# Kernel optimization log

Hardware: AMD Instinct MI355X
Metric: run time of the kernel (lower is better)

Reference implementation:

```python
import jax, jax.numpy as jnp
import numpy as np

EMBEDDING_LENGTH = 2048
EMBEDDING_DIM = 4


def setup_inputs() -> dict:
    key = jax.random.key(0)
    kx, ke = jax.random.split(key)
    x = jax.random.uniform(kx, (16, 64, 64, EMBEDDING_DIM), dtype=jnp.float32)
    embedding = jax.random.uniform(ke, (EMBEDDING_LENGTH, EMBEDDING_DIM), dtype=jnp.float32)
    return {"x": x, "embedding": embedding}


def reference(x, embedding):
    # x: [B, w, h, c], embedding: [K, c]
    B, w, h, c = x.shape
    flat = x.reshape(-1, c)  # [N, c], N = B*w*h
    # ||f - e||^2 = ||f||^2 - 2 f.e + ||e||^2 (avoids materializing [N, K, c])
    x2 = jnp.sum(flat * flat, axis=-1, keepdims=True)          # [N, 1]
    e2 = jnp.sum(embedding * embedding, axis=-1)               # [K]
    dots = jnp.einsum('nc,kc->nk', flat, embedding)            # [N, K]
    dists = x2 - 2.0 * dots + e2                               # [N, K]
    idx = jnp.argmin(dists, axis=-1)                           # [N] int
    return idx.reshape(B, w, h)
```

## Files before the change

kernel.cpp:

```cpp
#include <hip/hip_runtime.h>
#include <math.h>

#pragma clang fp contract(off)

typedef __attribute__((ext_vector_type(2))) float f2;

constexpr int KCODES = 2048;
constexpr int CDIM   = 4;
constexpr int KSPLIT = 8;
constexpr int KCHUNK = KCODES / KSPLIT;
constexpr int ROWS   = 64;
constexpr int NUNITS = KCODES / 2;

__device__ __forceinline__ f2 pk_mul(f2 a, f2 b) {
    f2 d; asm("v_pk_mul_f32 %0, %1, %2" : "=v"(d) : "v"(a), "v"(b)); return d;
}
__device__ __forceinline__ f2 pk_fma(f2 a, f2 b, f2 c) {
    f2 d; asm("v_pk_fma_f32 %0, %1, %2, %3" : "=v"(d) : "v"(a), "v"(b), "v"(c)); return d;
}
__device__ __forceinline__ f2 pk_add(f2 a, f2 b) {
    f2 d; asm("v_pk_add_f32 %0, %1, %2" : "=v"(d) : "v"(a), "v"(b)); return d;
}
__device__ __forceinline__ float min3f(float a, float b, float c) {
    float d; asm("v_min3_f32 %0, %1, %2, %3" : "=v"(d) : "v"(a), "v"(b), "v"(c)); return d;
}

__device__ __forceinline__ float sumsq(float4 e) {
    return ((e.x * e.x + e.y * e.y) + e.z * e.z) + e.w * e.w;
}

__global__ __launch_bounds__(512, 4) void vq_fused(
    const float* __restrict__ x,
    const float* __restrict__ emb,
    int* __restrict__ out,
    int N)
{
    __shared__ float4 sEP[NUNITS * 2];
    __shared__ float4 sSP[KCODES / 4];

    const float4* __restrict__ embf4 = reinterpret_cast<const float4*>(emb);
    const int t = threadIdx.x;

    for (int j = t; j < NUNITS; j += 512) {
        float4 a = embf4[2 * j], b = embf4[2 * j + 1];
        sEP[2 * j]     = make_float4(a.x, b.x, a.y, b.y);
        sEP[2 * j + 1] = make_float4(a.z, b.z, a.w, b.w);
    }
    for (int q = t; q < KCODES / 4; q += 512) {
        float4 e0 = embf4[4 * q], e1 = embf4[4 * q + 1];
        float4 e2 = embf4[4 * q + 2], e3 = embf4[4 * q + 3];
        sSP[q] = make_float4(sumsq(e0), sumsq(e1), sumsq(e2), sumsq(e3));
    }
    __syncthreads();

    const int lane = t & 63;
    const int n    = blockIdx.x * ROWS + lane;
    const int wid   = __builtin_amdgcn_readfirstlane(t >> 6);
    const int kbase = wid * KCHUNK;
    const int ubase = kbase >> 1;
    const int qbase = kbase >> 2;

    unsigned long long key = ~0ull;
    if (n < N) {
        const float4 xv = reinterpret_cast<const float4*>(x)[n];
        const float x2 = ((xv.x * xv.x + xv.y * xv.y) + xv.z * xv.z) + xv.w * xv.w;
        const f2 xx = {xv.x, xv.x}, yy = {xv.y, xv.y};
        const f2 zz = {xv.z, xv.z}, ww = {xv.w, xv.w};
        const f2 x2p = {x2, x2};
        const f2 m2  = {-2.0f, -2.0f};

        float dmin = HUGE_VALF;
        int bg = 0;

        for (int g = 0; g < KCHUNK / 8; ++g) {
            const float prev = dmin;
            const float4 sA = sSP[qbase + 2 * g];
            const float4 sB = sSP[qbase + 2 * g + 1];
            const int u0 = ubase + 4 * g;
            #pragma unroll
            for (int uu = 0; uu < 4; ++uu) {
                const float4 qa = sEP[2 * (u0 + uu)];
                const float4 qb = sEP[2 * (u0 + uu) + 1];
                const f2 sp = (uu == 0) ? f2{sA.x, sA.y} :
                              (uu == 1) ? f2{sA.z, sA.w} :
                              (uu == 2) ? f2{sB.x, sB.y} : f2{sB.z, sB.w};
                f2 dot = pk_mul(xx, f2{qa.x, qa.y});
                dot = pk_fma(yy, f2{qa.z, qa.w}, dot);
                dot = pk_fma(zz, f2{qb.x, qb.y}, dot);
                dot = pk_fma(ww, f2{qb.z, qb.w}, dot);
                f2 dd = pk_add(pk_fma(m2, dot, x2p), sp);
                dmin = min3f(dmin, dd.x, dd.y);
            }
            if (dmin < prev) bg = g;
        }

        const int k0 = kbase + (bg << 3);
        int idx = 0x7fffffff;
        #pragma unroll
        for (int r = 0; r < 8; ++r) {
            const int k = k0 + r;
            const float4 e = embf4[k];
            const float s = sumsq(e);
            float dot = xv.x * e.x;
            dot = __builtin_fmaf(xv.y, e.y, dot);
            dot = __builtin_fmaf(xv.z, e.z, dot);
            dot = __builtin_fmaf(xv.w, e.w, dot);
            const float d = __builtin_fmaf(-2.0f, dot, x2) + s;
            idx = min(idx, (d == dmin) ? k : 0x7fffffff);
        }

        key = ((unsigned long long)__float_as_uint(dmin) << 32) | (unsigned)idx;
    }

    __syncthreads();
    unsigned long long* skey = reinterpret_cast<unsigned long long*>(sEP);
    skey[lane * (KSPLIT + 1) + wid] = key;
    __syncthreads();

    if (t < ROWS) {
        const int rn = blockIdx.x * ROWS + t;
        if (rn < N) {
            unsigned long long k = skey[t * (KSPLIT + 1)];
            #pragma unroll
            for (int s = 1; s < KSPLIT; ++s) {
                unsigned long long v = skey[t * (KSPLIT + 1) + s];
                if (v < k) k = v;
            }
            out[rn] = (int)(unsigned)(k & 0xFFFFFFFFull);
        }
    }
}

extern "C" void kernel_launch(void* const* d_in, const int* in_sizes, int n_in,
                              void* d_out, int out_size, void* d_ws, size_t ws_size,
                              hipStream_t stream) {
    const float* x   = (const float*)d_in[0];
    const float* emb = (const float*)d_in[1];
    int* out = (int*)d_out;
    const int N = in_sizes[0] / CDIM;

    vq_fused<<<(N + ROWS - 1) / ROWS, 512, 0, stream>>>(x, emb, out, N);
}
```

Measured before the change: 30.59 us.

## Process four rows per thread to reuse codebook LDS loads

```diff
diff --git a/kernel.cpp b/kernel.cpp
--- a/kernel.cpp
+++ b/kernel.cpp
@@ -9,7 +9,8 @@
 constexpr int CDIM   = 4;
 constexpr int KSPLIT = 8;
 constexpr int KCHUNK = KCODES / KSPLIT;
-constexpr int ROWS   = 64;
+constexpr int RPT    = 4;
+constexpr int ROWSPB = 64 * RPT;
 constexpr int NUNITS = KCODES / 2;
 
 __device__ __forceinline__ f2 pk_mul(f2 a, f2 b) {
@@ -29,7 +30,7 @@
     return ((e.x * e.x + e.y * e.y) + e.z * e.z) + e.w * e.w;
 }
 
-__global__ __launch_bounds__(512, 4) void vq_fused(
+__global__ __launch_bounds__(512) void vq_fused(
     const float* __restrict__ x,
     const float* __restrict__ emb,
     int* __restrict__ out,
@@ -47,78 +48,98 @@
         sEP[2 * j + 1] = make_float4(a.z, b.z, a.w, b.w);
     }
     for (int q = t; q < KCODES / 4; q += 512) {
-        float4 e0 = embf4[4 * q], e1 = embf4[4 * q + 1];
+        float4 e0 = embf4[4 * q],     e1 = embf4[4 * q + 1];
         float4 e2 = embf4[4 * q + 2], e3 = embf4[4 * q + 3];
         sSP[q] = make_float4(sumsq(e0), sumsq(e1), sumsq(e2), sumsq(e3));
     }
     __syncthreads();
 
     const int lane = t & 63;
-    const int n    = blockIdx.x * ROWS + lane;
     const int wid   = __builtin_amdgcn_readfirstlane(t >> 6);
     const int kbase = wid * KCHUNK;
     const int ubase = kbase >> 1;
     const int qbase = kbase >> 2;
+    const int nbase = blockIdx.x * ROWSPB + lane;
 
-    unsigned long long key = ~0ull;
-    if (n < N) {
-        const float4 xv = reinterpret_cast<const float4*>(x)[n];
-        const float x2 = ((xv.x * xv.x + xv.y * xv.y) + xv.z * xv.z) + xv.w * xv.w;
-        const f2 xx = {xv.x, xv.x}, yy = {xv.y, xv.y};
-        const f2 zz = {xv.z, xv.z}, ww = {xv.w, xv.w};
-        const f2 x2p = {x2, x2};
-        const f2 m2  = {-2.0f, -2.0f};
+    float4 xv[RPT];
+    f2 xx[RPT], yy[RPT], zz[RPT], ww[RPT], x2p[RPT];
+    float dmin[RPT];
+    int   bg[RPT];
+    #pragma unroll
+    for (int r = 0; r < RPT; ++r) {
+        const int n = nbase + r * 64;
+        xv[r] = (n < N) ? reinterpret_cast<const float4*>(x)[n]
+                        : make_float4(0.f, 0.f, 0.f, 0.f);
+        const float x2 = ((xv[r].x * xv[r].x + xv[r].y * xv[r].y)
+                          + xv[r].z * xv[r].z) + xv[r].w * xv[r].w;
+        xx[r] = f2{xv[r].x, xv[r].x}; yy[r] = f2{xv[r].y, xv[r].y};
+        zz[r] = f2{xv[r].z, xv[r].z}; ww[r] = f2{xv[r].w, xv[r].w};
+        x2p[r] = f2{x2, x2};
+        dmin[r] = HUGE_VALF; bg[r] = 0;
+    }
+    const f2 m2 = {-2.0f, -2.0f};
 
-        float dmin = HUGE_VALF;
-        int bg = 0;
+    for (int g = 0; g < KCHUNK / 8; ++g) {
+        float prev[RPT];
+        #pragma unroll
+        for (int r = 0; r < RPT; ++r) prev[r] = dmin[r];
 
-        for (int g = 0; g < KCHUNK / 8; ++g) {
-            const float prev = dmin;
-            const float4 sA = sSP[qbase + 2 * g];
-            const float4 sB = sSP[qbase + 2 * g + 1];
-            const int u0 = ubase + 4 * g;
+        const float4 sA = sSP[qbase + 2 * g];
+        const float4 sB = sSP[qbase + 2 * g + 1];
+        const int u0 = ubase + 4 * g;
+        #pragma unroll
+        for (int uu = 0; uu < 4; ++uu) {
+            const float4 qa = sEP[2 * (u0 + uu)];
+            const float4 qb = sEP[2 * (u0 + uu) + 1];
+            const f2 ea = {qa.x, qa.y}, eb = {qa.z, qa.w};
+            const f2 ec = {qb.x, qb.y}, ed = {qb.z, qb.w};
+            const f2 sp = (uu == 0) ? f2{sA.x, sA.y} :
+                          (uu == 1) ? f2{sA.z, sA.w} :
+                          (uu == 2) ? f2{sB.x, sB.y} : f2{sB.z, sB.w};
             #pragma unroll
-            for (int uu = 0; uu < 4; ++uu) {
-                const float4 qa = sEP[2 * (u0 + uu)];
-                const float4 qb = sEP[2 * (u0 + uu) + 1];
-                const f2 sp = (uu == 0) ? f2{sA.x, sA.y} :
-                              (uu == 1) ? f2{sA.z, sA.w} :
-                              (uu == 2) ? f2{sB.x, sB.y} : f2{sB.z, sB.w};
-                f2 dot = pk_mul(xx, f2{qa.x, qa.y});
-                dot = pk_fma(yy, f2{qa.z, qa.w}, dot);
-                dot = pk_fma(zz, f2{qb.x, qb.y}, dot);
-                dot = pk_fma(ww, f2{qb.z, qb.w}, dot);
-                f2 dd = pk_add(pk_fma(m2, dot, x2p), sp);
-                dmin = min3f(dmin, dd.x, dd.y);
+            for (int r = 0; r < RPT; ++r) {
+                f2 dot = pk_mul(xx[r], ea);
+                dot = pk_fma(yy[r], eb, dot);
+                dot = pk_fma(zz[r], ec, dot);
+                dot = pk_fma(ww[r], ed, dot);
+                f2 dd = pk_add(pk_fma(m2, dot, x2p[r]), sp);
+                dmin[r] = min3f(dmin[r], dd.x, dd.y);
             }
-            if (dmin < prev) bg = g;
         }
+        #pragma unroll
+        for (int r = 0; r < RPT; ++r)
+            if (dmin[r] < prev[r]) bg[r] = g;
+    }
 
-        const int k0 = kbase + (bg << 3);
+    unsigned long long key[RPT];
+    #pragma unroll
+    for (int r = 0; r < RPT; ++r) {
+        const int k0 = kbase + (bg[r] << 3);
         int idx = 0x7fffffff;
         #pragma unroll
-        for (int r = 0; r < 8; ++r) {
-            const int k = k0 + r;
+        for (int q = 0; q < 8; ++q) {
+            const int k = k0 + q;
             const float4 e = embf4[k];
             const float s = sumsq(e);
-            float dot = xv.x * e.x;
-            dot = __builtin_fmaf(xv.y, e.y, dot);
-            dot = __builtin_fmaf(xv.z, e.z, dot);
-            dot = __builtin_fmaf(xv.w, e.w, dot);
-            const float d = __builtin_fmaf(-2.0f, dot, x2) + s;
-            idx = min(idx, (d == dmin) ? k : 0x7fffffff);
+            float dot = xv[r].x * e.x;
+            dot = __builtin_fmaf(xv[r].y, e.y, dot);
+            dot = __builtin_fmaf(xv[r].z, e.z, dot);
+            dot = __builtin_fmaf(xv[r].w, e.w, dot);
+            const float d = __builtin_fmaf(-2.0f, dot, x2p[r].x) + s;
+            idx = min(idx, (d == dmin[r]) ? k : 0x7fffffff);
         }
-
-        key = ((unsigned long long)__float_as_uint(dmin) << 32) | (unsigned)idx;
+        key[r] = ((unsigned long long)__float_as_uint(dmin[r]) << 32) | (unsigned)idx;
     }
 
     __syncthreads();
     unsigned long long* skey = reinterpret_cast<unsigned long long*>(sEP);
-    skey[lane * (KSPLIT + 1) + wid] = key;
+    #pragma unroll
+    for (int r = 0; r < RPT; ++r)
+        skey[(r * 64 + lane) * (KSPLIT + 1) + wid] = key[r];
     __syncthreads();
 
-    if (t < ROWS) {
-        const int rn = blockIdx.x * ROWS + t;
+    if (t < ROWSPB) {
+        const int rn = blockIdx.x * ROWSPB + t;
         if (rn < N) {
             unsigned long long k = skey[t * (KSPLIT + 1)];
             #pragma unroll
@@ -139,5 +160,5 @@
     int* out = (int*)d_out;
     const int N = in_sizes[0] / CDIM;
 
-    vq_fused<<<(N + ROWS - 1) / ROWS, 512, 0, stream>>>(x, emb, out, N);
+    vq_fused<<<(N + ROWSPB - 1) / ROWSPB, 512, 0, stream>>>(x, emb, out, N);
 }
```

New measurement: 30.20 us. No clear change (-1.3%).
